# Optimization experiments

Measured on AMD Instinct MI355X. Metric: run time of the kernel, lower is better.

## Reference

```python
import jax, jax.numpy as jnp
import numpy as np

N, E = 50000, 500000          # nodes, edges
IN_DIM = 128
HID = 128
T, R, H, L = 4, 5, 4, 2       # node types, edge types, heads, layers
DK = HID // H                 # per-head dim


def setup_inputs() -> dict:
    key = jax.random.key(0)
    ks = jax.random.split(key, 16)
    s = 0.05
    inp = {
        "node_feature": jax.random.normal(ks[0], (N, IN_DIM), jnp.float32),
        "node_type": jax.random.randint(ks[1], (N,), 0, T, jnp.int32),
        "edge_time": jax.random.randint(ks[2], (E,), 0, 128, jnp.int32),
        "edge_index": jax.random.randint(ks[3], (2, E), 0, N, jnp.int32),
        "edge_type": jax.random.randint(ks[4], (E,), 0, R, jnp.int32),
        # per-node-type input adaptation
        "adapt_w": jax.random.normal(ks[5], (T, IN_DIM, HID), jnp.float32) * s,
        "adapt_b": jnp.zeros((T, HID), jnp.float32),
        # HGT layer params, stacked over layers L and node types T
        "kw": jax.random.normal(ks[6], (L, T, HID, HID), jnp.float32) * s,
        "kb": jnp.zeros((L, T, HID), jnp.float32),
        "qw": jax.random.normal(ks[7], (L, T, HID, HID), jnp.float32) * s,
        "qb": jnp.zeros((L, T, HID), jnp.float32),
        "vw": jax.random.normal(ks[8], (L, T, HID, HID), jnp.float32) * s,
        "vb": jnp.zeros((L, T, HID), jnp.float32),
        "aw": jax.random.normal(ks[9], (L, T, HID, HID), jnp.float32) * s,
        "ab": jnp.zeros((L, T, HID), jnp.float32),
        # relation (edge-type) specific params
        "rel_pri": jnp.ones((L, R, H), jnp.float32),
        "rel_att": jax.random.normal(ks[10], (L, R, H, DK, DK), jnp.float32) * (1.0 / np.sqrt(DK)),
        "rel_msg": jax.random.normal(ks[11], (L, R, H, DK, DK), jnp.float32) * (1.0 / np.sqrt(DK)),
        "skip": jnp.ones((L, T), jnp.float32),
    }
    return inp


def _type_linear(x, types, W, b):
    # per-node-type linear: small fixed loop over T types, masked select
    out = jnp.zeros((x.shape[0], W.shape[-1]), x.dtype)
    for t in range(W.shape[0]):
        out = jnp.where((types == t)[:, None], x @ W[t] + b[t], out)
    return out


def _hgt_layer(x, node_type, src, dst, edge_type,
               kw, kb, qw, qb, vw, vb, aw, ab, rel_pri, rel_att, rel_msg, skip):
    n = x.shape[0]
    k = _type_linear(x, node_type, kw, kb).reshape(n, H, DK)
    q = _type_linear(x, node_type, qw, qb).reshape(n, H, DK)
    v = _type_linear(x, node_type, vw, vb).reshape(n, H, DK)
    ke, qe, ve = k[src], q[dst], v[src]              # [E,H,DK] gathers
    att = jnp.zeros((ke.shape[0], H), x.dtype)
    msg = jnp.zeros_like(ve)
    inv_sqrt_dk = np.float32(1.0 / np.sqrt(DK))
    for r in range(R):                                # small fixed loop over edge types
        m = edge_type == r
        kt = jnp.einsum('ehi,hij->ehj', ke, rel_att[r])
        a = (qe * kt).sum(-1) * rel_pri[r] * inv_sqrt_dk   # [E,H]
        mt = jnp.einsum('ehi,hij->ehj', ve, rel_msg[r])    # [E,H,DK]
        att = jnp.where(m[:, None], a, att)
        msg = jnp.where(m[:, None, None], mt, msg)
    # segment softmax over incoming edges of each destination node
    amax = jax.ops.segment_max(att, dst, num_segments=n)
    amax = jnp.where(jnp.isfinite(amax), amax, 0.0)
    ex = jnp.exp(att - amax[dst])
    den = jax.ops.segment_sum(ex, dst, num_segments=n)
    alpha = ex / jnp.maximum(den[dst], 1e-9)
    res = jax.ops.segment_sum(alpha[:, :, None] * msg, dst, num_segments=n).reshape(n, HID)
    # target-specific update with gated residual (HGT skip)
    trans = _type_linear(jax.nn.gelu(res), node_type, aw, ab)
    sk = jax.nn.sigmoid(skip)[node_type][:, None]
    return trans * sk + x * (1.0 - sk)


def reference(node_feature, node_type, edge_time, edge_index, edge_type,
              adapt_w, adapt_b, kw, kb, qw, qb, vw, vb, aw, ab,
              rel_pri, rel_att, rel_msg, skip):
    # per-type adapt -> tanh (dropout p=0 is identity)
    h = jnp.tanh(_type_linear(node_feature, node_type, adapt_w, adapt_b))
    src, dst = edge_index[0], edge_index[1]
    for l in range(L):
        h = _hgt_layer(h, node_type, src, dst, edge_type,
                       kw[l], kb[l], qw[l], qb[l], vw[l], vb[l], aw[l], ab[l],
                       rel_pri[l], rel_att[l], rel_msg[l], skip[l])
    return h
```

## Files before the change

kernel.cpp:

```cpp
#include <hip/hip_runtime.h>

#define T_NT 4
#define T_R  5
#define T_H  4
#define T_DK 32
#define T_HD 128
#define T_L  2
#define NCOL 1408

typedef unsigned short u16;
typedef __bf16 bf8_t __attribute__((ext_vector_type(8)));
typedef float f4_t __attribute__((ext_vector_type(4)));

__device__ __forceinline__ float bf2f(u16 u){
  union { float f; unsigned int i; } v; v.i = ((unsigned int)u) << 16; return v.f;
}
__device__ __forceinline__ float blo(unsigned u){
  union { float f; unsigned int i; } v; v.i = u << 16; return v.f;
}
__device__ __forceinline__ float bhi(unsigned u){
  union { float f; unsigned int i; } v; v.i = u & 0xffff0000u; return v.f;
}
__device__ __forceinline__ u16 f2bf(float f){
  union { float f; unsigned int i; } v; v.f = f;
  unsigned int x = v.i;
  return (u16)((x + 0x7fffu + ((x >> 16) & 1u)) >> 16);
}
__device__ __forceinline__ unsigned pk2(float a, float b){
  return (unsigned)f2bf(a) | ((unsigned)f2bf(b) << 16);
}
__device__ __forceinline__ float gelu_f(float x){
  float x3 = x*x*x;
  return 0.5f * x * (1.f + tanhf(0.7978845608028654f * (x + 0.044715f * x3)));
}
__device__ __forceinline__ int perm_l(int m){
  return (m & ~31) | ((m & 4) << 2) | ((m & 24) >> 1) | (m & 3);
}

__global__ void k_hist4(const int* __restrict__ key, int* __restrict__ cnt, int n){
  __shared__ int c[T_NT];
  int tid = threadIdx.x;
  if (tid < T_NT) c[tid] = 0;
  __syncthreads();
  int base = blockIdx.x*1024;
#pragma unroll
  for (int j=0;j<4;j++){
    int i = base + tid + j*256;
    if (i < n) atomicAdd(&c[key[i]], 1);
  }
  __syncthreads();
  if (tid < T_NT) atomicAdd(&cnt[tid], c[tid]);
}

__global__ void k_toff(const int* __restrict__ cnt, int* __restrict__ off, int* __restrict__ tcur){
  if (threadIdx.x == 0){
    off[0] = 0;
    for (int t = 0; t < T_NT; ++t) off[t+1] = off[t] + cnt[t];
    for (int t = 0; t < T_NT; ++t) tcur[t] = off[t];
  }
}

__global__ void k_scatter2(const int* __restrict__ nt, int* __restrict__ tcur,
                           int* __restrict__ perm, int* __restrict__ iperm, int n){
  __shared__ int lc[T_NT], lb[T_NT];
  int tid = threadIdx.x;
  if (tid < T_NT) lc[tid] = 0;
  __syncthreads();
  int base = blockIdx.x*1024;
  int t[4], lr[4];
#pragma unroll
  for (int j=0;j<4;j++){
    int i = base + tid + j*256;
    if (i < n){ t[j] = nt[i]; lr[j] = atomicAdd(&lc[t[j]], 1); }
    else t[j] = -1;
  }
  __syncthreads();
  if (tid < T_NT) lb[tid] = atomicAdd(&tcur[tid], lc[tid]);
  __syncthreads();
#pragma unroll
  for (int j=0;j<4;j++){
    if (t[j] >= 0){
      int node = base + tid + j*256;
      int pos = lb[t[j]] + lr[j];
      perm[pos] = node;
      iperm[node] = pos;
    }
  }
}

__global__ void k_deg(const int* __restrict__ dstp, const int* __restrict__ iperm,
                      int* __restrict__ degp, int* __restrict__ rank, int n){
  int i = blockIdx.x*256 + threadIdx.x;
  if (i < n) rank[i] = atomicAdd(&degp[(size_t)iperm[dstp[i]] << 4], 1);
}

__global__ void k_scanA(const int* __restrict__ degp, int* __restrict__ rp,
                        int* __restrict__ bsum, int n){
  __shared__ int buf[256];
  int tid = threadIdx.x;
  int i = blockIdx.x*256 + tid;
  int v = (i < n) ? degp[(size_t)i << 4] : 0;
  buf[tid] = v;
  __syncthreads();
  for (int off = 1; off < 256; off <<= 1){
    int add = (tid >= off) ? buf[tid - off] : 0;
    __syncthreads();
    buf[tid] += add;
    __syncthreads();
  }
  if (i < n) rp[i] = buf[tid] - v;
  if (tid == 255) bsum[blockIdx.x] = buf[255];
}
__global__ void k_scanB(int* __restrict__ bsum, int nb){
  __shared__ int buf[1024];
  int tid = threadIdx.x;
  int v = (tid < nb) ? bsum[tid] : 0;
  buf[tid] = v;
  __syncthreads();
  for (int off = 1; off < 1024; off <<= 1){
    int add = (tid >= off) ? buf[tid - off] : 0;
    __syncthreads();
    buf[tid] += add;
    __syncthreads();
  }
  if (tid < nb) bsum[tid] = buf[tid] - v;
}
__global__ void k_scanC(int* __restrict__ rp, const int* __restrict__ bsum,
                        int n, int E){
  int i = blockIdx.x*256 + threadIdx.x;
  if (i < n) rp[i] += bsum[blockIdx.x];
  if (i == 0) rp[n] = E;
}

__global__ void k_fill2(const int* __restrict__ srcp, const int* __restrict__ dstp,
                        const int* __restrict__ etp, const int* __restrict__ iperm,
                        const int* __restrict__ rp, const int* __restrict__ rank,
                        int* __restrict__ packed, int n){
  int i = blockIdx.x*256 + threadIdx.x;
  if (i < n){
    int d = iperm[dstp[i]];
    packed[rp[d] + rank[i]] = iperm[srcp[i]] | (etp[i] << 17);
  }
}

__global__ void k_prepmisc(const float* __restrict__ kw, const float* __restrict__ kb,
                           const float* __restrict__ qb, const float* __restrict__ vb,
                           const float* __restrict__ rel_att, const float* __restrict__ rel_msg,
                           const float* __restrict__ rel_pri,
                           u16* __restrict__ Ball, float* __restrict__ biasall)
{
  const float isd = 0.17677669529663687f;
  int idx = blockIdx.x*256 + threadIdx.x;
  if (idx < T_L*T_NT*T_HD*T_HD){
    int col = idx & 127, k = (idx >> 7) & 127, lt = idx >> 14;
    Ball[((size_t)lt*NCOL + col)*T_HD + k] = f2bf(kw[((size_t)lt*T_HD + k)*T_HD + col]);
    if (k == 0) biasall[(size_t)lt*NCOL + col] = kb[(size_t)lt*T_HD + col];
    return;
  }
  int b = idx - T_L*T_NT*T_HD*T_HD;
  if (b >= T_L*T_NT*1280) return;
  int lt = b / 1280, cc = b % 1280;
  int l = lt >> 2;
  int qv = cc >= 640, rem = cc - qv*640;
  int r = rem >> 7, hd = rem & 127, h = hd >> 5, o = hd & 31;
  float s = 0.f;
  if (!qv){
    const float* Ar = rel_att + ((((size_t)l*T_R + r)*T_H + h)*T_DK + o)*T_DK;
    const float* qbr = qb + (size_t)lt*T_HD + h*T_DK;
#pragma unroll
    for (int j = 0; j < 32; ++j) s += qbr[j] * Ar[j];
    s *= rel_pri[((size_t)l*T_R + r)*T_H + h] * isd;
  } else {
    const float* Mr = rel_msg + (((size_t)l*T_R + r)*T_H + h)*T_DK*T_DK + o;
    const float* vbr = vb + (size_t)lt*T_HD + h*T_DK;
#pragma unroll
    for (int i = 0; i < 32; ++i) s += vbr[i] * Mr[i*T_DK];
  }
  biasall[(size_t)lt*NCOL + 128 + qv*640 + r*128 + h*32 + o] = s;
}

__global__ __launch_bounds__(256)
void k_prepqv(const float* __restrict__ qw, const float* __restrict__ vw,
              const float* __restrict__ rel_att, const float* __restrict__ rel_msg,
              const float* __restrict__ rel_pri, u16* __restrict__ Ball)
{
  __shared__ float Ws[T_HD*33];
  __shared__ float As_[T_R*32*36];
  const float isd = 0.17677669529663687f;
  int h = blockIdx.x & 3, qv = blockIdx.x >> 2;
  int t = blockIdx.y, l = blockIdx.z;
  int lt = l*T_NT + t;
  int tid = threadIdx.x;
  const float* W = (qv ? vw : qw) + (size_t)lt*T_HD*T_HD;
  const float* rel = (qv ? rel_msg : rel_att);
#pragma unroll
  for (int i = 0; i < 16; ++i){
    int idx = tid + i*256;
    int j = idx & 31, k = idx >> 5;
    Ws[k*33 + j] = W[(size_t)k*T_HD + h*T_DK + j];
  }
#pragma unroll
  for (int i = 0; i < 20; ++i){
    int idx = tid + i*256;
    int bcol = idx & 31, a = (idx >> 5) & 31, r = idx >> 10;
    float wv = rel[((((size_t)l*T_R + r)*T_H + h)*T_DK + a)*T_DK + bcol];
    if (qv) As_[r*1152 + bcol*36 + a] = wv;
    else    As_[r*1152 + a*36 + bcol] = wv;
  }
  __syncthreads();
  int k = tid & 127, io = tid >> 7;
  float Wrow[32];
#pragma unroll
  for (int c = 0; c < 32; ++c) Wrow[c] = Ws[k*33 + c];
  for (int r = 0; r < T_R; ++r){
    float scale = qv ? 1.f : rel_pri[((size_t)l*T_R + r)*T_H + h] * isd;
#pragma unroll
    for (int i2 = 0; i2 < 16; ++i2){
      int o = i2*2 + io;
      const float4* ap = (const float4*)&As_[r*1152 + o*36];
      float acc = 0.f;
#pragma unroll
      for (int c4 = 0; c4 < 8; ++c4){
        float4 a4 = ap[c4];
        acc += Wrow[c4*4+0]*a4.x + Wrow[c4*4+1]*a4.y + Wrow[c4*4+2]*a4.z + Wrow[c4*4+3]*a4.w;
      }
      int col = 128 + qv*640 + r*128 + h*32 + o;
      Ball[((size_t)lt*NCOL + col)*T_HD + k] = f2bf(acc*scale);
    }
  }
}

__global__ void k_prepw2(const float* __restrict__ adapt_w, const float* __restrict__ aw,
                         u16* __restrict__ adaptT, u16* __restrict__ awT)
{
  int idx = blockIdx.x*256 + threadIdx.x;
  if (idx < T_NT*T_HD*T_HD){
    int k = idx & 127, col = (idx >> 7) & 127, t = idx >> 14;
    adaptT[idx] = f2bf(adapt_w[((size_t)t*T_HD + k)*T_HD + col]);
  } else {
    int j = idx - T_NT*T_HD*T_HD;
    if (j >= T_L*T_NT*T_HD*T_HD) return;
    int k = j & 127, col = (j >> 7) & 127, lt = j >> 14;
    awT[j] = f2bf(aw[((size_t)lt*T_HD + perm_l(k))*T_HD + col]);
  }
}

__global__ __launch_bounds__(256)
void k_qkvm(const float* __restrict__ X, const int* __restrict__ toff,
            const u16* __restrict__ Ball, const float* __restrict__ biasall,
            u16* __restrict__ kB, u16* __restrict__ qt, u16* __restrict__ mtp)
{
  __shared__ u16 As[64*128];
  int t = blockIdx.y;
  int z = blockIdx.z;
  int lo = toff[t], cnt = toff[t+1] - lo;
  int base = (int)blockIdx.x * 64;
  if (base >= cnt) return;
  int tid = threadIdx.x;
#pragma unroll
  for (int it = 0; it < 4; ++it){
    int chunk = tid + it*256;
    int row = chunk >> 4, c8 = (chunk & 15) << 3;
    uint4 o = make_uint4(0,0,0,0);
    if (base + row < cnt){
      const float* src = X + (size_t)(lo + base + row)*T_HD + c8;
      float4 f0 = *(const float4*)src;
      float4 f1 = *(const float4*)(src + 4);
      o.x = pk2(f0.x, f0.y);
      o.y = pk2(f0.z, f0.w);
      o.z = pk2(f1.x, f1.y);
      o.w = pk2(f1.z, f1.w);
    }
    int off16 = (row*128 + c8) ^ ((row & 7) << 3);
    *(uint4*)&As[off16] = o;
  }
  __syncthreads();

  int wid = tid >> 6, lane = tid & 63;
  int lr = lane & 15, lg = lane >> 4;
  bf8_t a[4][4];
#pragma unroll
  for (int rs = 0; rs < 4; ++rs)
#pragma unroll
    for (int kk = 0; kk < 4; ++kk){
      int row = rs*16 + lr;
      int off16 = (row*128 + kk*32 + lg*8) ^ ((row & 7) << 3);
      a[rs][kk] = *(const bf8_t*)&As[off16];
    }

  const u16* Bt = Ball + (size_t)t * NCOL * T_HD;
  const float* biast = biasall + (size_t)t * NCOL;

  int ci_end = z ? 44 : 22;
  for (int ci = z*22 + wid; ci < ci_end; ci += 4){
    int c0 = ci*2;
    int col0 = c0*16 + lr;
    const u16* bp0 = Bt + (size_t)col0*T_HD + lg*8;
    const u16* bp1 = bp0 + (size_t)16*T_HD;
    bf8_t b00 = *(const bf8_t*)(bp0);
    bf8_t b01 = *(const bf8_t*)(bp0 + 32);
    bf8_t b02 = *(const bf8_t*)(bp0 + 64);
    bf8_t b03 = *(const bf8_t*)(bp0 + 96);
    bf8_t b10 = *(const bf8_t*)(bp1);
    bf8_t b11 = *(const bf8_t*)(bp1 + 32);
    bf8_t b12 = *(const bf8_t*)(bp1 + 64);
    bf8_t b13 = *(const bf8_t*)(bp1 + 96);
    f4_t acc0[4], acc1[4];
#pragma unroll
    for (int rs = 0; rs < 4; ++rs){ acc0[rs] = (f4_t){0.f,0.f,0.f,0.f}; acc1[rs] = (f4_t){0.f,0.f,0.f,0.f}; }
#pragma unroll
    for (int rs = 0; rs < 4; ++rs){
      acc0[rs] = __builtin_amdgcn_mfma_f32_16x16x32_bf16(b00, a[rs][0], acc0[rs], 0, 0, 0);
      acc0[rs] = __builtin_amdgcn_mfma_f32_16x16x32_bf16(b01, a[rs][1], acc0[rs], 0, 0, 0);
      acc0[rs] = __builtin_amdgcn_mfma_f32_16x16x32_bf16(b02, a[rs][2], acc0[rs], 0, 0, 0);
      acc0[rs] = __builtin_amdgcn_mfma_f32_16x16x32_bf16(b03, a[rs][3], acc0[rs], 0, 0, 0);
      acc1[rs] = __builtin_amdgcn_mfma_f32_16x16x32_bf16(b10, a[rs][0], acc1[rs], 0, 0, 0);
      acc1[rs] = __builtin_amdgcn_mfma_f32_16x16x32_bf16(b11, a[rs][1], acc1[rs], 0, 0, 0);
      acc1[rs] = __builtin_amdgcn_mfma_f32_16x16x32_bf16(b12, a[rs][2], acc1[rs], 0, 0, 0);
      acc1[rs] = __builtin_amdgcn_mfma_f32_16x16x32_bf16(b13, a[rs][3], acc1[rs], 0, 0, 0);
    }
    float4 bias0 = *(const float4*)&biast[c0*16 + lg*4];
    float4 bias1 = *(const float4*)&biast[c0*16 + 16 + lg*4];
    int mco = ci*32 + lg*8;
    u16* dst; int cofs, stride;
    if (ci < 4)       { dst = kB;  cofs = mco;        stride = T_HD; }
    else if (ci < 24) { dst = qt;  cofs = mco - 128;  stride = T_R*T_HD; }
    else              { dst = mtp; cofs = mco - 768;  stride = T_R*T_HD; }
#pragma unroll
    for (int rs = 0; rs < 4; ++rs){
      int nl = rs*16 + lr;
      if (base + nl < cnt){
        uint4 o;
        o.x = pk2(acc0[rs][0] + bias0.x, acc0[rs][1] + bias0.y);
        o.y = pk2(acc0[rs][2] + bias0.z, acc0[rs][3] + bias0.w);
        o.z = pk2(acc1[rs][0] + bias1.x, acc1[rs][1] + bias1.y);
        o.w = pk2(acc1[rs][2] + bias1.z, acc1[rs][3] + bias1.w);
        *(uint4*)&dst[(size_t)(lo + base + nl)*stride + cofs] = o;
      }
    }
  }
}

template<int MODE, int GIN, int SOUT>
__global__ __launch_bounds__(256)
void k_ffn(const float* __restrict__ X, const int* __restrict__ tperm,
           const int* __restrict__ toff, const u16* __restrict__ WT,
           const float* __restrict__ Bi, float* __restrict__ outv,
           const float* __restrict__ h_in, const float* __restrict__ skipv)
{
  __shared__ u16 As[64*128];
  __shared__ int rows_s[64];
  int t = blockIdx.y;
  int lo = toff[t], cnt = toff[t+1] - lo;
  int base = (int)blockIdx.x * 64;
  if (base >= cnt) return;
  int tid = threadIdx.x;
  if (GIN || SOUT){
    if (tid < 64) rows_s[tid] = (base + tid < cnt) ? tperm[lo + base + tid] : 0;
    __syncthreads();
  }
#pragma unroll
  for (int it = 0; it < 4; ++it){
    int chunk = tid + it*256;
    int row = chunk >> 4, c8 = (chunk & 15) << 3;
    uint4 o = make_uint4(0,0,0,0);
    if (base + row < cnt){
      const float* src = GIN ? (X + (size_t)rows_s[row]*T_HD + c8)
                             : (X + (size_t)(lo + base + row)*T_HD + c8);
      float4 f0 = *(const float4*)src;
      float4 f1 = *(const float4*)(src + 4);
      if (MODE == 3){
        f0.x = gelu_f(f0.x); f0.y = gelu_f(f0.y); f0.z = gelu_f(f0.z); f0.w = gelu_f(f0.w);
        f1.x = gelu_f(f1.x); f1.y = gelu_f(f1.y); f1.z = gelu_f(f1.z); f1.w = gelu_f(f1.w);
      }
      o.x = pk2(f0.x, f0.y);
      o.y = pk2(f0.z, f0.w);
      o.z = pk2(f1.x, f1.y);
      o.w = pk2(f1.z, f1.w);
    }
    int off16 = (row*128 + c8) ^ ((row & 7) << 3);
    *(uint4*)&As[off16] = o;
  }
  __syncthreads();

  int wid = tid >> 6, lane = tid & 63;
  int lr = lane & 15, lg = lane >> 4;
  bf8_t a[4][4];
#pragma unroll
  for (int rs = 0; rs < 4; ++rs)
#pragma unroll
    for (int kk = 0; kk < 4; ++kk){
      int row = rs*16 + lr;
      int off16 = (row*128 + kk*32 + lg*8) ^ ((row & 7) << 3);
      a[rs][kk] = *(const bf8_t*)&As[off16];
    }

  const u16* Wt = WT + (size_t)t * T_HD * T_HD;
  float sk = 0.f;
  if (MODE == 3) sk = 1.f / (1.f + __expf(-skipv[t]));

  for (int c = wid; c < 8; c += 4){
    const u16* bp = Wt + (size_t)(c*16 + lr)*T_HD + lg*8;
    bf8_t b0 = *(const bf8_t*)(bp);
    bf8_t b1 = *(const bf8_t*)(bp + 32);
    bf8_t b2 = *(const bf8_t*)(bp + 64);
    bf8_t b3 = *(const bf8_t*)(bp + 96);
    f4_t acc[4];
#pragma unroll
    for (int rs = 0; rs < 4; ++rs) acc[rs] = (f4_t){0.f,0.f,0.f,0.f};
#pragma unroll
    for (int rs = 0; rs < 4; ++rs){
      acc[rs] = __builtin_amdgcn_mfma_f32_16x16x32_bf16(b0, a[rs][0], acc[rs], 0, 0, 0);
      acc[rs] = __builtin_amdgcn_mfma_f32_16x16x32_bf16(b1, a[rs][1], acc[rs], 0, 0, 0);
      acc[rs] = __builtin_amdgcn_mfma_f32_16x16x32_bf16(b2, a[rs][2], acc[rs], 0, 0, 0);
      acc[rs] = __builtin_amdgcn_mfma_f32_16x16x32_bf16(b3, a[rs][3], acc[rs], 0, 0, 0);
    }
    int cc = c*16 + lg*4;
    float4 bias4 = *(const float4*)&Bi[t*T_HD + cc];
#pragma unroll
    for (int rs = 0; rs < 4; ++rs){
      int nl = rs*16 + lr;
      if (base + nl < cnt){
        float4 vv;
        vv.x = acc[rs][0] + bias4.x;
        vv.y = acc[rs][1] + bias4.y;
        vv.z = acc[rs][2] + bias4.z;
        vv.w = acc[rs][3] + bias4.w;
        if (MODE == 1){
          vv.x = tanhf(vv.x); vv.y = tanhf(vv.y); vv.z = tanhf(vv.z); vv.w = tanhf(vv.w);
        }
        if (MODE == 3){
          float4 hr = *(const float4*)&h_in[(size_t)(lo + base + nl)*T_HD + cc];
          float osk = 1.f - sk;
          vv.x = vv.x*sk + hr.x*osk;
          vv.y = vv.y*sk + hr.y*osk;
          vv.z = vv.z*sk + hr.z*osk;
          vv.w = vv.w*sk + hr.w*osk;
        }
        size_t opos = SOUT ? (size_t)rows_s[nl] : (size_t)(lo + base + nl);
        *(float4*)&outv[opos*T_HD + cc] = vv;
      }
    }
  }
}

__global__ __launch_bounds__(256)
void k_edge_attn2(const u16* __restrict__ kB, const u16* __restrict__ qt,
                  const u16* __restrict__ mtp, const int* __restrict__ rp,
                  const int* __restrict__ packed, float* __restrict__ resb, int n)
{
  int lane = threadIdx.x & 63;
  int wid = (int)blockIdx.x * (blockDim.x >> 6) + (threadIdx.x >> 6);
  int nw = (int)gridDim.x * (blockDim.x >> 6);
  int l2 = lane << 1;
  for (int dst = wid; dst < n; dst += nw){
    int e0 = rp[dst], e1 = rp[dst+1];
    if (e0 == e1){
      *(float2*)&resb[(size_t)dst*T_HD + l2] = make_float2(0.f, 0.f);
      continue;
    }
    const u16* qrow = qt + (size_t)dst*(T_R*T_HD) + l2;
    float mA=-INFINITY, dA=0.f, aA0=0.f, aA1=0.f;
    float mB=-INFINITY, dB=0.f, aB0=0.f, aB1=0.f;
    int ei = e0;
    for (; ei + 1 < e1; ei += 2){
      int pka = packed[ei], pkb = packed[ei+1];
      int sa = pka & 131071, ra = pka >> 17;
      int sb = pkb & 131071, rb = pkb >> 17;
      unsigned ka = *(const unsigned*)&kB[(sa << 7) + l2];
      unsigned kb = *(const unsigned*)&kB[(sb << 7) + l2];
      unsigned qa = *(const unsigned*)&qrow[ra << 7];
      unsigned qb = *(const unsigned*)&qrow[rb << 7];
      unsigned ma = *(const unsigned*)&mtp[((sa*T_R + ra) << 7) + l2];
      unsigned mb = *(const unsigned*)&mtp[((sb*T_R + rb) << 7) + l2];
      float pa = blo(qa)*blo(ka) + bhi(qa)*bhi(ka);
      float pb = blo(qb)*blo(kb) + bhi(qb)*bhi(kb);
      pa += __shfl_xor(pa, 1);  pb += __shfl_xor(pb, 1);
      pa += __shfl_xor(pa, 2);  pb += __shfl_xor(pb, 2);
      pa += __shfl_xor(pa, 4);  pb += __shfl_xor(pb, 4);
      pa += __shfl_xor(pa, 8);  pb += __shfl_xor(pb, 8);
      float mnA = fmaxf(mA, pa), mnB = fmaxf(mB, pb);
      float scA = __expf(mA - mnA), scB = __expf(mB - mnB);
      float wA = __expf(pa - mnA),  wB = __expf(pb - mnB);
      mA = mnA; mB = mnB;
      dA  = dA*scA + wA;          dB  = dB*scB + wB;
      aA0 = aA0*scA + wA*blo(ma); aB0 = aB0*scB + wB*blo(mb);
      aA1 = aA1*scA + wA*bhi(ma); aB1 = aB1*scB + wB*bhi(mb);
    }
    if (ei < e1){
      int pka = packed[ei];
      int sa = pka & 131071, ra = pka >> 17;
      unsigned ka = *(const unsigned*)&kB[(sa << 7) + l2];
      unsigned qa = *(const unsigned*)&qrow[ra << 7];
      unsigned ma = *(const unsigned*)&mtp[((sa*T_R + ra) << 7) + l2];
      float pa = blo(qa)*blo(ka) + bhi(qa)*bhi(ka);
      pa += __shfl_xor(pa, 1);
      pa += __shfl_xor(pa, 2);
      pa += __shfl_xor(pa, 4);
      pa += __shfl_xor(pa, 8);
      float mnA = fmaxf(mA, pa);
      float scA = __expf(mA - mnA);
      float wA = __expf(pa - mnA);
      mA = mnA;
      dA  = dA*scA + wA;
      aA0 = aA0*scA + wA*blo(ma);
      aA1 = aA1*scA + wA*bhi(ma);
    }
    float mn = fmaxf(mA, mB);
    float eA = __expf(mA - mn), eB = __expf(mB - mn);
    float d  = dA*eA + dB*eB;
    float a0 = aA0*eA + aB0*eB;
    float a1 = aA1*eA + aB1*eB;
    float inv = 1.f / fmaxf(d, 1e-9f);
    *(float2*)&resb[(size_t)dst*T_HD + l2] = make_float2(a0*inv, a1*inv);
  }
}

extern "C" void kernel_launch(void* const* d_in, const int* in_sizes, int n_in,
                              void* d_out, int out_size, void* d_ws, size_t ws_size,
                              hipStream_t stream)
{
  const float* node_feature = (const float*)d_in[0];
  const int* node_type    = (const int*)d_in[1];
  const int* edge_index   = (const int*)d_in[3];
  const int* edge_type    = (const int*)d_in[4];
  const float* adapt_w = (const float*)d_in[5];
  const float* adapt_b = (const float*)d_in[6];
  const float* kw = (const float*)d_in[7];
  const float* kb = (const float*)d_in[8];
  const float* qw = (const float*)d_in[9];
  const float* qb = (const float*)d_in[10];
  const float* vw = (const float*)d_in[11];
  const float* vb = (const float*)d_in[12];
  const float* aw = (const float*)d_in[13];
  const float* ab = (const float*)d_in[14];
  const float* rel_pri = (const float*)d_in[15];
  const float* rel_att = (const float*)d_in[16];
  const float* rel_msg = (const float*)d_in[17];
  const float* skipp   = (const float*)d_in[18];

  const int N = in_sizes[1];
  const int E = in_sizes[4];
  const int* srcp = edge_index;
  const int* dstp = edge_index + E;

  char* p = (char*)d_ws;
  auto take = [&](size_t bytes)->char*{
    char* r = p; p += (bytes + 255) & ~(size_t)255; return r;
  };
  float* h0   = (float*)take((size_t)N*T_HD*4);
  float* resb = (float*)take((size_t)N*T_HD*4);
  u16*  kB    = (u16*) take((size_t)N*T_HD*2);
  u16*  qt    = (u16*) take((size_t)N*T_R*T_HD*2);
  u16*  mtp   = (u16*) take((size_t)N*T_R*T_HD*2);
  u16*  Ball  = (u16*) take((size_t)T_L*T_NT*NCOL*T_HD*2);
  float* biasall = (float*)take((size_t)T_L*T_NT*NCOL*4);
  u16*  adaptT = (u16*)take((size_t)T_NT*T_HD*T_HD*2);
  u16*  awT    = (u16*)take((size_t)T_L*T_NT*T_HD*T_HD*2);
  int* degp   = (int*) take((size_t)N*16*4);
  int* rp     = (int*) take(((size_t)N+1)*4);
  int* rank   = (int*) take((size_t)E*4);
  int* packed = (int*) take((size_t)E*4);
  int* tcnt   = (int*) take(256);
  int* toff   = (int*) take(256);
  int* tcur   = (int*) take(256);
  int* bsum   = (int*) take(1024);
  int* tperm  = (int*) take((size_t)N*4);
  int* iperm  = (int*) take((size_t)N*4);

  hipMemsetAsync(degp, 0, (size_t)N*16*4, stream);
  hipMemsetAsync(tcnt, 0, 256, stream);

  int nb_n4 = (N + 1023)/1024, nb_e = (E + 255)/256;
  int nb_s  = (N + 255)/256;
  k_hist4<<<nb_n4, 256, 0, stream>>>(node_type, tcnt, N);
  k_toff<<<1, 64, 0, stream>>>(tcnt, toff, tcur);
  k_scatter2<<<nb_n4, 256, 0, stream>>>(node_type, tcur, tperm, iperm, N);
  k_deg<<<nb_e, 256, 0, stream>>>(dstp, iperm, degp, rank, E);
  k_scanA<<<nb_s, 256, 0, stream>>>(degp, rp, bsum, N);
  k_scanB<<<1, 1024, 0, stream>>>(bsum, nb_s);
  k_scanC<<<nb_s, 256, 0, stream>>>(rp, bsum, N, E);
  k_fill2<<<nb_e, 256, 0, stream>>>(srcp, dstp, edge_type, iperm, rp, rank, packed, E);

  int misc_total = T_L*T_NT*T_HD*T_HD + T_L*T_NT*1280;
  k_prepmisc<<<(misc_total + 255)/256, 256, 0, stream>>>(
      kw, kb, qb, vb, rel_att, rel_msg, rel_pri, Ball, biasall);
  k_prepqv<<<dim3(8, T_NT, T_L), 256, 0, stream>>>(
      qw, vw, rel_att, rel_msg, rel_pri, Ball);
  int w2_total = T_NT*T_HD*T_HD + T_L*T_NT*T_HD*T_HD;
  k_prepw2<<<(w2_total + 255)/256, 256, 0, stream>>>(adapt_w, aw, adaptT, awT);

  dim3 gg((N + 63)/64, T_NT);
  dim3 gq((N + 63)/64, T_NT, 2);
  k_ffn<1,1,0><<<gg, 256, 0, stream>>>(node_feature, tperm, toff, adaptT, adapt_b, h0, nullptr, nullptr);

  for (int l = 0; l < T_L; ++l){
    size_t bo = (size_t)l * T_NT * T_HD;
    k_qkvm<<<gq, 256, 0, stream>>>(h0, toff,
        Ball + (size_t)l*T_NT*NCOL*T_HD, biasall + (size_t)l*T_NT*NCOL,
        kB, qt, mtp);
    k_edge_attn2<<<2048, 256, 0, stream>>>(kB, qt, mtp, rp, packed, resb, N);
    if (l == T_L - 1)
      k_ffn<3,0,1><<<gg, 256, 0, stream>>>(resb, tperm, toff,
          awT + (size_t)l*T_NT*T_HD*T_HD, ab + bo, (float*)d_out, h0, skipp + l*T_NT);
    else
      k_ffn<3,0,0><<<gg, 256, 0, stream>>>(resb, tperm, toff,
          awT + (size_t)l*T_NT*T_HD*T_HD, ab + bo, h0, h0, skipp + l*T_NT);
  }
}
```

Measured before the change: 392.9 us.

## Defer relation message transform past aggregation; gather plain V per edge

The per-relation message projection is no longer applied to V for every (node, relation) pair. Instead, attention weights accumulate plain V separately per relation into a 5x128 bf16 buffer per destination node, and a new FFN kernel multiplies this by a stacked block-diagonal rel_msg matrix before GELU and the output projection. This cuts the QKV GEMM columns from 1408 to 896 and shrinks the per-edge gather from a 5x-wide message tensor to one V row. The online softmax also now rescales only when the running max grows by more than 8, which is checked per wave. The costs are five accumulator pairs per lane with a switch on the edge type, an extra 640-deep GEMM per node, and a bf16 intermediate.

```diff
diff --git a/kernel.cpp b/kernel.cpp
--- a/kernel.cpp
+++ b/kernel.cpp
@@ -6,15 +6,12 @@
 #define T_DK 32
 #define T_HD 128
 #define T_L  2
-#define NCOL 1408
+#define NCOL 896
 
 typedef unsigned short u16;
 typedef __bf16 bf8_t __attribute__((ext_vector_type(8)));
 typedef float f4_t __attribute__((ext_vector_type(4)));
 
-__device__ __forceinline__ float bf2f(u16 u){
-  union { float f; unsigned int i; } v; v.i = ((unsigned int)u) << 16; return v.f;
-}
 __device__ __forceinline__ float blo(unsigned u){
   union { float f; unsigned int i; } v; v.i = u << 16; return v.f;
 }
@@ -144,55 +141,53 @@
 }
 
 __global__ void k_prepmisc(const float* __restrict__ kw, const float* __restrict__ kb,
-                           const float* __restrict__ qb, const float* __restrict__ vb,
-                           const float* __restrict__ rel_att, const float* __restrict__ rel_msg,
-                           const float* __restrict__ rel_pri,
+                           const float* __restrict__ vw, const float* __restrict__ vb,
+                           const float* __restrict__ qb,
+                           const float* __restrict__ rel_att, const float* __restrict__ rel_pri,
                            u16* __restrict__ Ball, float* __restrict__ biasall)
 {
   const float isd = 0.17677669529663687f;
+  const int KPART = T_L*T_NT*T_HD*T_HD;
   int idx = blockIdx.x*256 + threadIdx.x;
-  if (idx < T_L*T_NT*T_HD*T_HD){
+  if (idx < KPART){
     int col = idx & 127, k = (idx >> 7) & 127, lt = idx >> 14;
     Ball[((size_t)lt*NCOL + col)*T_HD + k] = f2bf(kw[((size_t)lt*T_HD + k)*T_HD + col]);
     if (k == 0) biasall[(size_t)lt*NCOL + col] = kb[(size_t)lt*T_HD + col];
     return;
   }
-  int b = idx - T_L*T_NT*T_HD*T_HD;
-  if (b >= T_L*T_NT*1280) return;
-  int lt = b / 1280, cc = b % 1280;
+  if (idx < 2*KPART){
+    int j = idx - KPART;
+    int col = j & 127, k = (j >> 7) & 127, lt = j >> 14;
+    Ball[((size_t)lt*NCOL + 768 + col)*T_HD + k] = f2bf(vw[((size_t)lt*T_HD + k)*T_HD + col]);
+    if (k == 0) biasall[(size_t)lt*NCOL + 768 + col] = vb[(size_t)lt*T_HD + col];
+    return;
+  }
+  int b = idx - 2*KPART;
+  if (b >= T_L*T_NT*640) return;
+  int lt = b / 640, cc = b % 640;
   int l = lt >> 2;
-  int qv = cc >= 640, rem = cc - qv*640;
-  int r = rem >> 7, hd = rem & 127, h = hd >> 5, o = hd & 31;
+  int r = cc >> 7, hd = cc & 127, h = hd >> 5, o = hd & 31;
+  const float* Ar = rel_att + ((((size_t)l*T_R + r)*T_H + h)*T_DK + o)*T_DK;
+  const float* qbr = qb + (size_t)lt*T_HD + h*T_DK;
   float s = 0.f;
-  if (!qv){
-    const float* Ar = rel_att + ((((size_t)l*T_R + r)*T_H + h)*T_DK + o)*T_DK;
-    const float* qbr = qb + (size_t)lt*T_HD + h*T_DK;
-#pragma unroll
-    for (int j = 0; j < 32; ++j) s += qbr[j] * Ar[j];
-    s *= rel_pri[((size_t)l*T_R + r)*T_H + h] * isd;
-  } else {
-    const float* Mr = rel_msg + (((size_t)l*T_R + r)*T_H + h)*T_DK*T_DK + o;
-    const float* vbr = vb + (size_t)lt*T_HD + h*T_DK;
-#pragma unroll
-    for (int i = 0; i < 32; ++i) s += vbr[i] * Mr[i*T_DK];
-  }
-  biasall[(size_t)lt*NCOL + 128 + qv*640 + r*128 + h*32 + o] = s;
+#pragma unroll
+  for (int j = 0; j < 32; ++j) s += qbr[j] * Ar[j];
+  s *= rel_pri[((size_t)l*T_R + r)*T_H + h] * isd;
+  biasall[(size_t)lt*NCOL + 128 + cc] = s;
 }
 
 __global__ __launch_bounds__(256)
-void k_prepqv(const float* __restrict__ qw, const float* __restrict__ vw,
-              const float* __restrict__ rel_att, const float* __restrict__ rel_msg,
+void k_prepqv(const float* __restrict__ qw, const float* __restrict__ rel_att,
               const float* __restrict__ rel_pri, u16* __restrict__ Ball)
 {
   __shared__ float Ws[T_HD*33];
   __shared__ float As_[T_R*32*36];
   const float isd = 0.17677669529663687f;
-  int h = blockIdx.x & 3, qv = blockIdx.x >> 2;
+  int h = blockIdx.x;
   int t = blockIdx.y, l = blockIdx.z;
   int lt = l*T_NT + t;
   int tid = threadIdx.x;
-  const float* W = (qv ? vw : qw) + (size_t)lt*T_HD*T_HD;
-  const float* rel = (qv ? rel_msg : rel_att);
+  const float* W = qw + (size_t)lt*T_HD*T_HD;
 #pragma unroll
   for (int i = 0; i < 16; ++i){
     int idx = tid + i*256;
@@ -203,9 +198,7 @@
   for (int i = 0; i < 20; ++i){
     int idx = tid + i*256;
     int bcol = idx & 31, a = (idx >> 5) & 31, r = idx >> 10;
-    float wv = rel[((((size_t)l*T_R + r)*T_H + h)*T_DK + a)*T_DK + bcol];
-    if (qv) As_[r*1152 + bcol*36 + a] = wv;
-    else    As_[r*1152 + a*36 + bcol] = wv;
+    As_[r*1152 + a*36 + bcol] = rel_att[((((size_t)l*T_R + r)*T_H + h)*T_DK + a)*T_DK + bcol];
   }
   __syncthreads();
   int k = tid & 127, io = tid >> 7;
@@ -213,7 +206,7 @@
 #pragma unroll
   for (int c = 0; c < 32; ++c) Wrow[c] = Ws[k*33 + c];
   for (int r = 0; r < T_R; ++r){
-    float scale = qv ? 1.f : rel_pri[((size_t)l*T_R + r)*T_H + h] * isd;
+    float scale = rel_pri[((size_t)l*T_R + r)*T_H + h] * isd;
 #pragma unroll
     for (int i2 = 0; i2 < 16; ++i2){
       int o = i2*2 + io;
@@ -224,10 +217,23 @@
         float4 a4 = ap[c4];
         acc += Wrow[c4*4+0]*a4.x + Wrow[c4*4+1]*a4.y + Wrow[c4*4+2]*a4.z + Wrow[c4*4+3]*a4.w;
       }
-      int col = 128 + qv*640 + r*128 + h*32 + o;
+      int col = 128 + r*128 + h*32 + o;
       Ball[((size_t)lt*NCOL + col)*T_HD + k] = f2bf(acc*scale);
     }
   }
+}
+
+__global__ void k_prepW2(const float* __restrict__ rel_msg, u16* __restrict__ W2T){
+  int idx = blockIdx.x*256 + threadIdx.x;
+  if (idx >= T_L*128*640) return;
+  int l = idx / (128*640), rem = idx % (128*640);
+  int outcol = rem / 640, kidx = rem % 640;
+  int r = kidx >> 7, pd = kidx & 127;
+  int ld = perm_l(pd);
+  int h = ld >> 5, i = ld & 31;
+  int ho = outcol >> 5, j = outcol & 31;
+  float v = (h == ho) ? rel_msg[((((size_t)l*T_R + r)*T_H + h)*T_DK + i)*T_DK + j] : 0.f;
+  W2T[idx] = f2bf(v);
 }
 
 __global__ void k_prepw2(const float* __restrict__ adapt_w, const float* __restrict__ aw,
@@ -241,14 +247,14 @@
     int j = idx - T_NT*T_HD*T_HD;
     if (j >= T_L*T_NT*T_HD*T_HD) return;
     int k = j & 127, col = (j >> 7) & 127, lt = j >> 14;
-    awT[j] = f2bf(aw[((size_t)lt*T_HD + perm_l(k))*T_HD + col]);
+    awT[j] = f2bf(aw[((size_t)lt*T_HD + k)*T_HD + col]);
   }
 }
 
 __global__ __launch_bounds__(256)
 void k_qkvm(const float* __restrict__ X, const int* __restrict__ toff,
             const u16* __restrict__ Ball, const float* __restrict__ biasall,
-            u16* __restrict__ kB, u16* __restrict__ qt, u16* __restrict__ mtp)
+            u16* __restrict__ kB, u16* __restrict__ qt, u16* __restrict__ vB)
 {
   __shared__ u16 As[64*128];
   int t = blockIdx.y;
@@ -291,8 +297,8 @@
   const u16* Bt = Ball + (size_t)t * NCOL * T_HD;
   const float* biast = biasall + (size_t)t * NCOL;
 
-  int ci_end = z ? 44 : 22;
-  for (int ci = z*22 + wid; ci < ci_end; ci += 4){
+  int ci_end = z ? 28 : 14;
+  for (int ci = z*14 + wid; ci < ci_end; ci += 4){
     int c0 = ci*2;
     int col0 = c0*16 + lr;
     const u16* bp0 = Bt + (size_t)col0*T_HD + lg*8;
@@ -325,7 +331,7 @@
     u16* dst; int cofs, stride;
     if (ci < 4)       { dst = kB;  cofs = mco;        stride = T_HD; }
     else if (ci < 24) { dst = qt;  cofs = mco - 128;  stride = T_R*T_HD; }
-    else              { dst = mtp; cofs = mco - 768;  stride = T_R*T_HD; }
+    else              { dst = vB;  cofs = mco - 768;  stride = T_HD; }
 #pragma unroll
     for (int rs = 0; rs < 4; ++rs){
       int nl = rs*16 + lr;
@@ -369,10 +375,6 @@
                              : (X + (size_t)(lo + base + row)*T_HD + c8);
       float4 f0 = *(const float4*)src;
       float4 f1 = *(const float4*)(src + 4);
-      if (MODE == 3){
-        f0.x = gelu_f(f0.x); f0.y = gelu_f(f0.y); f0.z = gelu_f(f0.z); f0.w = gelu_f(f0.w);
-        f1.x = gelu_f(f1.x); f1.y = gelu_f(f1.y); f1.z = gelu_f(f1.z); f1.w = gelu_f(f1.w);
-      }
       o.x = pk2(f0.x, f0.y);
       o.y = pk2(f0.z, f0.w);
       o.z = pk2(f1.x, f1.y);
@@ -396,9 +398,6 @@
     }
 
   const u16* Wt = WT + (size_t)t * T_HD * T_HD;
-  float sk = 0.f;
-  if (MODE == 3) sk = 1.f / (1.f + __expf(-skipv[t]));
-
   for (int c = wid; c < 8; c += 4){
     const u16* bp = Wt + (size_t)(c*16 + lr)*T_HD + lg*8;
     bf8_t b0 = *(const bf8_t*)(bp);
@@ -422,21 +421,10 @@
       int nl = rs*16 + lr;
       if (base + nl < cnt){
         float4 vv;
-        vv.x = acc[rs][0] + bias4.x;
-        vv.y = acc[rs][1] + bias4.y;
-        vv.z = acc[rs][2] + bias4.z;
-        vv.w = acc[rs][3] + bias4.w;
-        if (MODE == 1){
-          vv.x = tanhf(vv.x); vv.y = tanhf(vv.y); vv.z = tanhf(vv.z); vv.w = tanhf(vv.w);
-        }
-        if (MODE == 3){
-          float4 hr = *(const float4*)&h_in[(size_t)(lo + base + nl)*T_HD + cc];
-          float osk = 1.f - sk;
-          vv.x = vv.x*sk + hr.x*osk;
-          vv.y = vv.y*sk + hr.y*osk;
-          vv.z = vv.z*sk + hr.z*osk;
-          vv.w = vv.w*sk + hr.w*osk;
-        }
+        vv.x = tanhf(acc[rs][0] + bias4.x);
+        vv.y = tanhf(acc[rs][1] + bias4.y);
+        vv.z = tanhf(acc[rs][2] + bias4.z);
+        vv.w = tanhf(acc[rs][3] + bias4.w);
         size_t opos = SOUT ? (size_t)rows_s[nl] : (size_t)(lo + base + nl);
         *(float4*)&outv[opos*T_HD + cc] = vv;
       }
@@ -444,10 +432,123 @@
   }
 }
 
+template<int SOUT>
 __global__ __launch_bounds__(256)
-void k_edge_attn2(const u16* __restrict__ kB, const u16* __restrict__ qt,
-                  const u16* __restrict__ mtp, const int* __restrict__ rp,
-                  const int* __restrict__ packed, float* __restrict__ resb, int n)
+void k_ffn2(const u16* __restrict__ S, const int* __restrict__ tperm,
+            const int* __restrict__ toff, const u16* __restrict__ W2T,
+            const u16* __restrict__ awT, const float* __restrict__ Bi,
+            float* __restrict__ outv, const float* __restrict__ h_in,
+            const float* __restrict__ skipv)
+{
+  __shared__ u16 Rs[64*128];
+  __shared__ int rows_s[64];
+  int t = blockIdx.y;
+  int lo = toff[t], cnt = toff[t+1] - lo;
+  int base = (int)blockIdx.x * 64;
+  if (base >= cnt) return;
+  int tid = threadIdx.x;
+  if (SOUT){
+    if (tid < 64) rows_s[tid] = (base + tid < cnt) ? tperm[lo + base + tid] : 0;
+  }
+  __syncthreads();
+  int wid = tid >> 6, lane = tid & 63;
+  int lr = lane & 15, lg = lane >> 4;
+
+  f4_t acc[2][4];
+#pragma unroll
+  for (int ch = 0; ch < 2; ++ch)
+#pragma unroll
+    for (int rs = 0; rs < 4; ++rs) acc[ch][rs] = (f4_t){0.f,0.f,0.f,0.f};
+  for (int r = 0; r < T_R; ++r){
+    bf8_t a[4][4];
+#pragma unroll
+    for (int rs = 0; rs < 4; ++rs)
+#pragma unroll
+      for (int kk = 0; kk < 4; ++kk)
+        a[rs][kk] = *(const bf8_t*)&S[(size_t)(lo + base + rs*16 + lr)*(T_R*T_HD) + r*T_HD + kk*32 + lg*8];
+#pragma unroll
+    for (int ch = 0; ch < 2; ++ch){
+      int c = wid*2 + ch;
+      const u16* bp = W2T + (size_t)(c*16 + lr)*640 + r*T_HD + lg*8;
+      bf8_t b0 = *(const bf8_t*)(bp);
+      bf8_t b1 = *(const bf8_t*)(bp + 32);
+      bf8_t b2 = *(const bf8_t*)(bp + 64);
+      bf8_t b3 = *(const bf8_t*)(bp + 96);
+#pragma unroll
+      for (int rs = 0; rs < 4; ++rs){
+        acc[ch][rs] = __builtin_amdgcn_mfma_f32_16x16x32_bf16(b0, a[rs][0], acc[ch][rs], 0, 0, 0);
+        acc[ch][rs] = __builtin_amdgcn_mfma_f32_16x16x32_bf16(b1, a[rs][1], acc[ch][rs], 0, 0, 0);
+        acc[ch][rs] = __builtin_amdgcn_mfma_f32_16x16x32_bf16(b2, a[rs][2], acc[ch][rs], 0, 0, 0);
+        acc[ch][rs] = __builtin_amdgcn_mfma_f32_16x16x32_bf16(b3, a[rs][3], acc[ch][rs], 0, 0, 0);
+      }
+    }
+  }
+#pragma unroll
+  for (int ch = 0; ch < 2; ++ch){
+    int col = (wid*2 + ch)*16 + lg*4;
+#pragma unroll
+    for (int rs = 0; rs < 4; ++rs){
+      int node = rs*16 + lr;
+      uint2 o;
+      o.x = pk2(gelu_f(acc[ch][rs][0]), gelu_f(acc[ch][rs][1]));
+      o.y = pk2(gelu_f(acc[ch][rs][2]), gelu_f(acc[ch][rs][3]));
+      int off16 = (node*128 + col) ^ ((node & 7) << 3);
+      *(uint2*)&Rs[off16] = o;
+    }
+  }
+  __syncthreads();
+
+  bf8_t a2[4][4];
+#pragma unroll
+  for (int rs = 0; rs < 4; ++rs)
+#pragma unroll
+    for (int kk = 0; kk < 4; ++kk){
+      int row = rs*16 + lr;
+      int off16 = (row*128 + kk*32 + lg*8) ^ ((row & 7) << 3);
+      a2[rs][kk] = *(const bf8_t*)&Rs[off16];
+    }
+  const u16* Wt = awT + (size_t)t * T_HD * T_HD;
+  float sk = 1.f / (1.f + __expf(-skipv[t]));
+  float osk = 1.f - sk;
+  for (int c = wid; c < 8; c += 4){
+    const u16* bp = Wt + (size_t)(c*16 + lr)*T_HD + lg*8;
+    bf8_t b0 = *(const bf8_t*)(bp);
+    bf8_t b1 = *(const bf8_t*)(bp + 32);
+    bf8_t b2 = *(const bf8_t*)(bp + 64);
+    bf8_t b3 = *(const bf8_t*)(bp + 96);
+    f4_t ac[4];
+#pragma unroll
+    for (int rs = 0; rs < 4; ++rs) ac[rs] = (f4_t){0.f,0.f,0.f,0.f};
+#pragma unroll
+    for (int rs = 0; rs < 4; ++rs){
+      ac[rs] = __builtin_amdgcn_mfma_f32_16x16x32_bf16(b0, a2[rs][0], ac[rs], 0, 0, 0);
+      ac[rs] = __builtin_amdgcn_mfma_f32_16x16x32_bf16(b1, a2[rs][1], ac[rs], 0, 0, 0);
+      ac[rs] = __builtin_amdgcn_mfma_f32_16x16x32_bf16(b2, a2[rs][2], ac[rs], 0, 0, 0);
+      ac[rs] = __builtin_amdgcn_mfma_f32_16x16x32_bf16(b3, a2[rs][3], ac[rs], 0, 0, 0);
+    }
+    int cc = c*16 + lg*4;
+    float4 bias4 = *(const float4*)&Bi[t*T_HD + cc];
+#pragma unroll
+    for (int rs = 0; rs < 4; ++rs){
+      int nl = rs*16 + lr;
+      if (base + nl < cnt){
+        float4 hr = *(const float4*)&h_in[(size_t)(lo + base + nl)*T_HD + cc];
+        float4 vv;
+        vv.x = (ac[rs][0] + bias4.x)*sk + hr.x*osk;
+        vv.y = (ac[rs][1] + bias4.y)*sk + hr.y*osk;
+        vv.z = (ac[rs][2] + bias4.z)*sk + hr.z*osk;
+        vv.w = (ac[rs][3] + bias4.w)*sk + hr.w*osk;
+        size_t opos = SOUT ? (size_t)rows_s[nl] : (size_t)(lo + base + nl);
+        *(float4*)&outv[opos*T_HD + cc] = vv;
+      }
+    }
+  }
+}
+
+__global__ __launch_bounds__(256)
+void k_edge_attn3(const u16* __restrict__ kB, const u16* __restrict__ qt,
+                  const u16* __restrict__ vB, const int* __restrict__ rp,
+                  const int* __restrict__ packed, u16* __restrict__ S, int n)
 {
   int lane = threadIdx.x & 63;
   int wid = (int)blockIdx.x * (blockDim.x >> 6) + (threadIdx.x >> 6);
@@ -455,64 +556,73 @@
   int l2 = lane << 1;
   for (int dst = wid; dst < n; dst += nw){
     int e0 = rp[dst], e1 = rp[dst+1];
-    if (e0 == e1){
-      *(float2*)&resb[(size_t)dst*T_HD + l2] = make_float2(0.f, 0.f);
-      continue;
-    }
     const u16* qrow = qt + (size_t)dst*(T_R*T_HD) + l2;
-    float mA=-INFINITY, dA=0.f, aA0=0.f, aA1=0.f;
-    float mB=-INFINITY, dB=0.f, aB0=0.f, aB1=0.f;
+    float m = -1e30f, d = 0.f;
+    float a00=0.f,a01=0.f,a10=0.f,a11=0.f,a20=0.f,a21=0.f,a30=0.f,a31=0.f,a40=0.f,a41=0.f;
+#define RESCALE(sc) { d*=sc; a00*=sc;a01*=sc;a10*=sc;a11*=sc;a20*=sc;a21*=sc;a30*=sc;a31*=sc;a40*=sc;a41*=sc; }
+#define ACCUM(rr, w, vv) { float v0=(w)*blo(vv), v1=(w)*bhi(vv); \
+      switch(rr){ case 0: a00+=v0; a01+=v1; break; case 1: a10+=v0; a11+=v1; break; \
+                  case 2: a20+=v0; a21+=v1; break; case 3: a30+=v0; a31+=v1; break; \
+                  default: a40+=v0; a41+=v1; break; } }
     int ei = e0;
     for (; ei + 1 < e1; ei += 2){
       int pka = packed[ei], pkb = packed[ei+1];
       int sa = pka & 131071, ra = pka >> 17;
       int sb = pkb & 131071, rb = pkb >> 17;
       unsigned ka = *(const unsigned*)&kB[(sa << 7) + l2];
-      unsigned kb = *(const unsigned*)&kB[(sb << 7) + l2];
+      unsigned kbv = *(const unsigned*)&kB[(sb << 7) + l2];
       unsigned qa = *(const unsigned*)&qrow[ra << 7];
       unsigned qb = *(const unsigned*)&qrow[rb << 7];
-      unsigned ma = *(const unsigned*)&mtp[((sa*T_R + ra) << 7) + l2];
-      unsigned mb = *(const unsigned*)&mtp[((sb*T_R + rb) << 7) + l2];
+      unsigned va = *(const unsigned*)&vB[(sa << 7) + l2];
+      unsigned vbv = *(const unsigned*)&vB[(sb << 7) + l2];
       float pa = blo(qa)*blo(ka) + bhi(qa)*bhi(ka);
-      float pb = blo(qb)*blo(kb) + bhi(qb)*bhi(kb);
+      float pb = blo(qb)*blo(kbv) + bhi(qb)*bhi(kbv);
       pa += __shfl_xor(pa, 1);  pb += __shfl_xor(pb, 1);
       pa += __shfl_xor(pa, 2);  pb += __shfl_xor(pb, 2);
       pa += __shfl_xor(pa, 4);  pb += __shfl_xor(pb, 4);
       pa += __shfl_xor(pa, 8);  pb += __shfl_xor(pb, 8);
-      float mnA = fmaxf(mA, pa), mnB = fmaxf(mB, pb);
-      float scA = __expf(mA - mnA), scB = __expf(mB - mnB);
-      float wA = __expf(pa - mnA),  wB = __expf(pb - mnB);
-      mA = mnA; mB = mnB;
-      dA  = dA*scA + wA;          dB  = dB*scB + wB;
-      aA0 = aA0*scA + wA*blo(ma); aB0 = aB0*scB + wB*blo(mb);
-      aA1 = aA1*scA + wA*bhi(ma); aB1 = aB1*scB + wB*bhi(mb);
+      float pmax = fmaxf(pa, pb);
+      if (__any(pmax > m + 8.f)){
+        float mn = fmaxf(m, pmax);
+        float sc = __expf(m - mn);
+        RESCALE(sc);
+        m = mn;
+      }
+      float wA = __expf(pa - m), wB = __expf(pb - m);
+      d += wA + wB;
+      ACCUM(ra, wA, va);
+      ACCUM(rb, wB, vbv);
     }
     if (ei < e1){
       int pka = packed[ei];
       int sa = pka & 131071, ra = pka >> 17;
       unsigned ka = *(const unsigned*)&kB[(sa << 7) + l2];
       unsigned qa = *(const unsigned*)&qrow[ra << 7];
-      unsigned ma = *(const unsigned*)&mtp[((sa*T_R + ra) << 7) + l2];
+      unsigned va = *(const unsigned*)&vB[(sa << 7) + l2];
       float pa = blo(qa)*blo(ka) + bhi(qa)*bhi(ka);
       pa += __shfl_xor(pa, 1);
       pa += __shfl_xor(pa, 2);
       pa += __shfl_xor(pa, 4);
       pa += __shfl_xor(pa, 8);
-      float mnA = fmaxf(mA, pa);
-      float scA = __expf(mA - mnA);
-      float wA = __expf(pa - mnA);
-      mA = mnA;
-      dA  = dA*scA + wA;
-      aA0 = aA0*scA + wA*blo(ma);
-      aA1 = aA1*scA + wA*bhi(ma);
-    }
-    float mn = fmaxf(mA, mB);
-    float eA = __expf(mA - mn), eB = __expf(mB - mn);
-    float d  = dA*eA + dB*eB;
-    float a0 = aA0*eA + aB0*eB;
-    float a1 = aA1*eA + aB1*eB;
+      if (__any(pa > m + 8.f)){
+        float mn = fmaxf(m, pa);
+        float sc = __expf(m - mn);
+        RESCALE(sc);
+        m = mn;
+      }
+      float wA = __expf(pa - m);
+      d += wA;
+      ACCUM(ra, wA, va);
+    }
+#undef RESCALE
+#undef ACCUM
     float inv = 1.f / fmaxf(d, 1e-9f);
-    *(float2*)&resb[(size_t)dst*T_HD + l2] = make_float2(a0*inv, a1*inv);
+    u16* srow = S + (size_t)dst*(T_R*T_HD) + l2;
+    *(unsigned*)&srow[0]   = pk2(a00*inv, a01*inv);
+    *(unsigned*)&srow[128] = pk2(a10*inv, a11*inv);
+    *(unsigned*)&srow[256] = pk2(a20*inv, a21*inv);
+    *(unsigned*)&srow[384] = pk2(a30*inv, a31*inv);
+    *(unsigned*)&srow[512] = pk2(a40*inv, a41*inv);
   }
 }
 
@@ -549,14 +659,15 @@
     char* r = p; p += (bytes + 255) & ~(size_t)255; return r;
   };
   float* h0   = (float*)take((size_t)N*T_HD*4);
-  float* resb = (float*)take((size_t)N*T_HD*4);
   u16*  kB    = (u16*) take((size_t)N*T_HD*2);
+  u16*  vB    = (u16*) take((size_t)N*T_HD*2);
   u16*  qt    = (u16*) take((size_t)N*T_R*T_HD*2);
-  u16*  mtp   = (u16*) take((size_t)N*T_R*T_HD*2);
+  u16*  S     = (u16*) take((size_t)(N+64)*T_R*T_HD*2);
   u16*  Ball  = (u16*) take((size_t)T_L*T_NT*NCOL*T_HD*2);
   float* biasall = (float*)take((size_t)T_L*T_NT*NCOL*4);
   u16*  adaptT = (u16*)take((size_t)T_NT*T_HD*T_HD*2);
   u16*  awT    = (u16*)take((size_t)T_L*T_NT*T_HD*T_HD*2);
+  u16*  W2T    = (u16*)take((size_t)T_L*T_HD*640*2);
   int* degp   = (int*) take((size_t)N*16*4);
   int* rp     = (int*) take(((size_t)N+1)*4);
   int* rank   = (int*) take((size_t)E*4);
@@ -582,11 +693,11 @@
   k_scanC<<<nb_s, 256, 0, stream>>>(rp, bsum, N, E);
   k_fill2<<<nb_e, 256, 0, stream>>>(srcp, dstp, edge_type, iperm, rp, rank, packed, E);
 
-  int misc_total = T_L*T_NT*T_HD*T_HD + T_L*T_NT*1280;
+  int misc_total = 2*T_L*T_NT*T_HD*T_HD + T_L*T_NT*640;
   k_prepmisc<<<(misc_total + 255)/256, 256, 0, stream>>>(
-      kw, kb, qb, vb, rel_att, rel_msg, rel_pri, Ball, biasall);
-  k_prepqv<<<dim3(8, T_NT, T_L), 256, 0, stream>>>(
-      qw, vw, rel_att, rel_msg, rel_pri, Ball);
+      kw, kb, vw, vb, qb, rel_att, rel_pri, Ball, biasall);
+  k_prepqv<<<dim3(4, T_NT, T_L), 256, 0, stream>>>(qw, rel_att, rel_pri, Ball);
+  k_prepW2<<<(T_L*128*640 + 255)/256, 256, 0, stream>>>(rel_msg, W2T);
   int w2_total = T_NT*T_HD*T_HD + T_L*T_NT*T_HD*T_HD;
   k_prepw2<<<(w2_total + 255)/256, 256, 0, stream>>>(adapt_w, aw, adaptT, awT);
 
@@ -598,13 +709,15 @@
     size_t bo = (size_t)l * T_NT * T_HD;
     k_qkvm<<<gq, 256, 0, stream>>>(h0, toff,
         Ball + (size_t)l*T_NT*NCOL*T_HD, biasall + (size_t)l*T_NT*NCOL,
-        kB, qt, mtp);
-    k_edge_attn2<<<2048, 256, 0, stream>>>(kB, qt, mtp, rp, packed, resb, N);
+        kB, qt, vB);
+    k_edge_attn3<<<2048, 256, 0, stream>>>(kB, qt, vB, rp, packed, S, N);
     if (l == T_L - 1)
-      k_ffn<3,0,1><<<gg, 256, 0, stream>>>(resb, tperm, toff,
-          awT + (size_t)l*T_NT*T_HD*T_HD, ab + bo, (float*)d_out, h0, skipp + l*T_NT);
+      k_ffn2<1><<<gg, 256, 0, stream>>>(S, tperm, toff,
+          W2T + (size_t)l*T_HD*640, awT + (size_t)l*T_NT*T_HD*T_HD, ab + bo,
+          (float*)d_out, h0, skipp + l*T_NT);
     else
-      k_ffn<3,0,0><<<gg, 256, 0, stream>>>(resb, tperm, toff,
-          awT + (size_t)l*T_NT*T_HD*T_HD, ab + bo, h0, h0, skipp + l*T_NT);
-  }
-}
+      k_ffn2<0><<<gg, 256, 0, stream>>>(S, tperm, toff,
+          W2T + (size_t)l*T_HD*640, awT + (size_t)l*T_NT*T_HD*T_HD, ab + bo,
+          h0, h0, skipp + l*T_NT);
+  }
+}
```

After: 478.3 us. 1.22x slower.
